# Optimization experiments

Hardware: AMD Instinct MI355X
Metric: run time of the kernel (lower is better)

The kernel has to match this reference:

```python
import jax, jax.numpy as jnp
import numpy as np

B = 16384
FEAT_SIZES = [1000000, 1000000, 500000, 500000, 100000, 100000, 10000, 10000]
EMB_DIM = 50          # min(50, feat_size//2) for all chosen sizes
CONT_IN = 64
D = 8 * EMB_DIM + 64  # 464 = total_embedding_size + 64
H1, H2 = 256, 128     # expert/cross hidden sizes
E, T = 4, 3           # num_experts, num_tasks


def setup_inputs() -> dict:
    key = jax.random.key(0)
    ks = iter(jax.random.split(key, 64))
    s = 0.02
    inp = {}
    inp["discrete_features"] = jax.random.randint(next(ks), (B, 8), 0, 10000)
    inp["continuous_features"] = jax.random.normal(next(ks), (B, CONT_IN), jnp.float32)
    for i, fs in enumerate(FEAT_SIZES):
        inp[f"emb{i}"] = jax.random.normal(next(ks), (fs, EMB_DIM), jnp.float32) * s
    inp["cont_W"] = jax.random.normal(next(ks), (CONT_IN, 64), jnp.float32) * s
    inp["cont_b"] = jnp.zeros((64,), jnp.float32)
    inp["fm_W"] = jax.random.normal(next(ks), (D, 10), jnp.float32) * s
    inp["cW1"] = jax.random.normal(next(ks), (D, H1), jnp.float32) * s
    inp["cb1"] = jnp.zeros((H1,), jnp.float32)
    inp["cW2"] = jax.random.normal(next(ks), (H1, H2), jnp.float32) * s
    inp["cb2"] = jnp.zeros((H2,), jnp.float32)
    inp["coW"] = jax.random.normal(next(ks), (H2, D), jnp.float32) * s
    inp["cob"] = jnp.zeros((D,), jnp.float32)
    inp["expW1"] = jax.random.normal(next(ks), (E, D, H1), jnp.float32) * s
    inp["expb1"] = jnp.zeros((E, H1), jnp.float32)
    inp["expW2"] = jax.random.normal(next(ks), (E, H1, H2), jnp.float32) * s
    inp["expb2"] = jnp.zeros((E, H2), jnp.float32)
    inp["gate_W"] = jax.random.normal(next(ks), (T, D, E), jnp.float32) * s
    inp["gate_b"] = jnp.zeros((T, E), jnp.float32)
    inp["task_W"] = jax.random.normal(next(ks), (T, H2, 1), jnp.float32) * s
    inp["task_b"] = jnp.zeros((T, 1), jnp.float32)
    inp["log_vars"] = jnp.zeros((T,), jnp.float32)
    return inp


def reference(discrete_features, continuous_features,
              emb0, emb1, emb2, emb3, emb4, emb5, emb6, emb7,
              cont_W, cont_b, fm_W, cW1, cb1, cW2, cb2, coW, cob,
              expW1, expb1, expW2, expb2, gate_W, gate_b,
              task_W, task_b, log_vars):
    tables = [emb0, emb1, emb2, emb3, emb4, emb5, emb6, emb7]
    embs = [jnp.take(t, discrete_features[:, i], axis=0) for i, t in enumerate(tables)]
    cont = jax.nn.relu(continuous_features @ cont_W + cont_b)           # [B,64]
    x = jnp.concatenate(embs + [cont], axis=1)                          # [B,D]
    # FM part: x @ fm_embedding.weight -> [B,10], square-of-sum minus sum-of-square
    xe = x @ fm_W
    fm = 0.5 * (jnp.sum(xe, 1, keepdims=True) ** 2
                - jnp.sum(xe ** 2, 1, keepdims=True))                   # [B,1]
    # cross network
    c = jax.nn.relu(x @ cW1 + cb1)
    c = jax.nn.relu(c @ cW2 + cb2)
    co = c @ coW + cob                                                  # [B,D]
    h = x + co + fm                                                     # [B,D] (fm broadcast)
    # experts as batched GEMMs: [B,E,H2]
    e1 = jax.nn.relu(jnp.einsum('bd,edh->beh', h, expW1) + expb1)
    eo = jnp.einsum('beh,eho->beo', e1, expW2) + expb2
    # gates: [B,T,E] softmax over experts
    g = jax.nn.softmax(jnp.einsum('bd,tde->bte', h, gate_W) + gate_b, axis=-1)
    mixed = jnp.einsum('bte,beo->bto', g, eo)                           # [B,T,H2]
    out = jnp.einsum('bto,tok->btk', mixed, task_W) + task_b            # [B,T,1]
    return out[..., 0], log_vars                                        # ([B,3], [3])
```

## Files before the change

### kernel.cpp

```cpp
#include <hip/hip_runtime.h>
#include <stdint.h>

typedef _Float16 f16;
typedef __attribute__((ext_vector_type(8))) _Float16 f16x8;
typedef __attribute__((ext_vector_type(4))) float    f32x4;

constexpr int BROWS = 16384;
constexpr int NTASK = 3;

constexpr int OFF_CW1 = 0;
constexpr int OFF_CW2 = OFF_CW1 + 256 * 480;
constexpr int OFF_COW = OFF_CW2 + 128 * 256;
constexpr int OFF_EW1 = OFF_COW + 512 * 128;
constexpr int OFF_EW2 = OFF_EW1 + 1024 * 480;
constexpr int OFF_FMW = OFF_EW2 + 512 * 256;
constexpr int OFF_GW  = OFF_FMW + 16 * 480;
constexpr int OFF_CTW = OFF_GW  + 16 * 480;
constexpr int PACK_TOTAL = OFF_CTW + 64 * 64;

__global__ __launch_bounds__(256)
void pack_all(const float* __restrict__ cW1, const float* __restrict__ cW2,
              const float* __restrict__ coW, const float* __restrict__ expW1,
              const float* __restrict__ expW2, const float* __restrict__ fmW,
              const float* __restrict__ gateW, const float* __restrict__ contW,
              f16* __restrict__ wp)
{
    const int idx = blockIdx.x * 256 + threadIdx.x;
    if (idx >= PACK_TOTAL) return;
    float v = 0.f;
    if (idx < OFF_CW2) {
        const int l = idx - OFF_CW1, n = l / 480, k = l % 480;
        if (k < 464) v = cW1[k * 256 + n];
    } else if (idx < OFF_COW) {
        const int l = idx - OFF_CW2, n = l / 256, k = l % 256;
        v = cW2[k * 128 + n];
    } else if (idx < OFF_EW1) {
        const int l = idx - OFF_COW, n = l / 128, k = l % 128;
        if (n < 464) v = coW[k * 464 + n];
    } else if (idx < OFF_EW2) {
        const int l = idx - OFF_EW1, n = l / 480, k = l % 480;
        const int e = n >> 8, nn = n & 255;
        if (k < 464) v = expW1[(e * 464 + k) * 256 + nn];
    } else if (idx < OFF_FMW) {
        const int l = idx - OFF_EW2, n = l / 256, k = l % 256;
        const int e = n >> 7, nn = n & 127;
        v = expW2[(e * 256 + k) * 128 + nn];
    } else if (idx < OFF_GW) {
        const int l = idx - OFF_FMW, c = l / 480, k = l % 480;
        if (c < 10 && k < 464) v = fmW[k * 10 + c];
    } else if (idx < OFF_CTW) {
        const int l = idx - OFF_GW, c = l / 480, k = l % 480;
        if (c < 12 && k < 464) {
            const int tt = c >> 2, e = c & 3;
            v = gateW[(tt * 464 + k) * 4 + e];
        }
    } else {
        const int l = idx - OFF_CTW, n = l / 64, k = l % 64;
        v = contW[k * 64 + n];
    }
    wp[idx] = (f16)v;
}

template<int MF, int NF, int KS, int LDA>
__device__ __forceinline__ void wave_gemm(
    const f16* __restrict__ As, int arow0,
    const f16* __restrict__ Bg, int bcol0, int ldb,
    f32x4 (&acc)[MF][NF], int lane)
{
    const int g = lane >> 4, rr = lane & 15;
#pragma unroll
    for (int kb = 0; kb < KS; ++kb) {
        const int ko = kb * 32 + g * 8;
        f16x8 bf[NF];
#pragma unroll
        for (int j = 0; j < NF; ++j)
            bf[j] = *(const f16x8*)(Bg + (long)(bcol0 + j * 16 + rr) * ldb + ko);
#pragma unroll
        for (int i = 0; i < MF; ++i) {
            const f16x8 af = *(const f16x8*)(As + (arow0 + i * 16 + rr) * LDA + ko);
#pragma unroll
            for (int j = 0; j < NF; ++j)
                acc[i][j] = __builtin_amdgcn_mfma_f32_16x16x32_f16(
                    af, bf[j], acc[i][j], 0, 0, 0);
        }
    }
}

__global__ __launch_bounds__(512, 1)
void mmoe_fused(const int* __restrict__ disc, const float* __restrict__ cf,
                const float* __restrict__ e0p, const float* __restrict__ e1p,
                const float* __restrict__ e2p, const float* __restrict__ e3p,
                const float* __restrict__ e4p, const float* __restrict__ e5p,
                const float* __restrict__ e6p, const float* __restrict__ e7p,
                const float* __restrict__ contB, const float* __restrict__ cb1,
                const float* __restrict__ cb2, const float* __restrict__ cob,
                const float* __restrict__ expb1, const float* __restrict__ expb2,
                const float* __restrict__ gateB, const float* __restrict__ taskW,
                const float* __restrict__ taskB, const float* __restrict__ logv,
                const f16* __restrict__ wp, float* __restrict__ out)
{
    __shared__ f16   sh_x [64][488];
    __shared__ f16   sh_c1[64][264];
    __shared__ f16   sh_c2[64][136];
    __shared__ float sh_g [64][12];
    __shared__ float sh_part[8][64][3];
    __shared__ float sh_fm[64];
    __shared__ const float* stabs[8];

    const int t = threadIdx.x;
    const int lane = t & 63, wave = t >> 6;
    const int g = lane >> 4, rr = lane & 15;
    const long r0 = (long)blockIdx.x * 64;

    const f16* cW1p = wp + OFF_CW1;
    const f16* cW2p = wp + OFF_CW2;
    const f16* coWp = wp + OFF_COW;
    const f16* eW1p = wp + OFF_EW1;
    const f16* eW2p = wp + OFF_EW2;
    const f16* fmWp = wp + OFF_FMW;
    const f16* gWp  = wp + OFF_GW;
    const f16* ctWp = wp + OFF_CTW;

    if (t == 0) {
        stabs[0] = e0p; stabs[1] = e1p; stabs[2] = e2p; stabs[3] = e3p;
        stabs[4] = e4p; stabs[5] = e5p; stabs[6] = e6p; stabs[7] = e7p;
    }
    __syncthreads();

    f16* cfp = (f16*)&sh_c2[0][0];
    for (int i = t; i < 64 * 24; i += 512) sh_x[i / 24][464 + i % 24] = (f16)0.f;
    {
        const int r = t >> 3, tab = t & 7;
        const long fi = disc[(r0 + r) * 8 + tab];
        const float* src = stabs[tab] + fi * 50;
        f16* dst = &sh_x[r][tab * 50];
#pragma unroll
        for (int q = 0; q < 25; ++q) {
            const float2 v = *(const float2*)(src + q * 2);
            dst[q * 2] = (f16)v.x; dst[q * 2 + 1] = (f16)v.y;
        }
    }
    for (int i = t; i < 64 * 16; i += 512) {
        const int r = i >> 4, q = i & 15;
        const float4 v = *(const float4*)(cf + (r0 + r) * 64 + q * 4);
        f16* dst = cfp + r * 72 + q * 4;
        dst[0] = (f16)v.x; dst[1] = (f16)v.y; dst[2] = (f16)v.z; dst[3] = (f16)v.w;
    }
    __syncthreads();

    {
        const int wm = wave >> 2, wn = wave & 3;
        f32x4 acc[2][1] = {};
        wave_gemm<2, 1, 2, 72>(cfp, wm * 32, ctWp, wn * 16, 64, acc, lane);
        const int col = wn * 16 + rr;
        const float bv = contB[col];
#pragma unroll
        for (int i = 0; i < 2; ++i)
#pragma unroll
            for (int rx = 0; rx < 4; ++rx)
                sh_x[wm * 32 + i * 16 + g * 4 + rx][400 + col] =
                    (f16)fmaxf(acc[i][0][rx] + bv, 0.f);
    }
    __syncthreads();

    if (wave < 4) {
        f32x4 a[1][1] = {};
        wave_gemm<1, 1, 15, 488>(&sh_x[0][0], wave * 16, fmWp, 0, 480, a, lane);
#pragma unroll
        for (int rx = 0; rx < 4; ++rx) {
            const float v = a[0][0][rx];
            float s = v, ss = v * v;
#pragma unroll
            for (int off = 1; off < 16; off <<= 1) {
                s += __shfl_xor(s, off, 64); ss += __shfl_xor(ss, off, 64);
            }
            if (rr == 0) sh_fm[wave * 16 + g * 4 + rx] = 0.5f * (s * s - ss);
        }
    }
    {
        f32x4 acc[4][2] = {};
        wave_gemm<4, 2, 15, 488>(&sh_x[0][0], 0, cW1p, wave * 32, 480, acc, lane);
#pragma unroll
        for (int j = 0; j < 2; ++j) {
            const int col = wave * 32 + j * 16 + rr;
            const float bv = cb1[col];
#pragma unroll
            for (int i = 0; i < 4; ++i)
#pragma unroll
                for (int rx = 0; rx < 4; ++rx)
                    sh_c1[i * 16 + g * 4 + rx][col] =
                        (f16)fmaxf(acc[i][j][rx] + bv, 0.f);
        }
    }
    __syncthreads();

    {
        f32x4 acc[4][1] = {};
        wave_gemm<4, 1, 8, 264>(&sh_c1[0][0], 0, cW2p, wave * 16, 256, acc, lane);
        const int col = wave * 16 + rr;
        const float bv = cb2[col];
#pragma unroll
        for (int i = 0; i < 4; ++i)
#pragma unroll
            for (int rx = 0; rx < 4; ++rx)
                sh_c2[i * 16 + g * 4 + rx][col] =
                    (f16)fmaxf(acc[i][0][rx] + bv, 0.f);
    }
    __syncthreads();

    {
        f32x4 acc[4][4] = {};
        wave_gemm<4, 4, 4, 136>(&sh_c2[0][0], 0, coWp, wave * 64, 128, acc, lane);
#pragma unroll
        for (int j = 0; j < 4; ++j) {
            const int col = wave * 64 + j * 16 + rr;
            if (col < 464) {
                const float bv = cob[col];
#pragma unroll
                for (int i = 0; i < 4; ++i)
#pragma unroll
                    for (int rx = 0; rx < 4; ++rx) {
                        const int row = i * 16 + g * 4 + rx;
                        const float v = acc[i][j][rx] + bv +
                                        (float)sh_x[row][col] + sh_fm[row];
                        sh_x[row][col] = (f16)v;
                    }
            }
        }
    }
    __syncthreads();

    if (wave < 4) {
        f32x4 a[1][1] = {};
        wave_gemm<1, 1, 15, 488>(&sh_x[0][0], wave * 16, gWp, 0, 480, a, lane);
        const float gb = (rr < 12) ? gateB[rr] : 0.f;
#pragma unroll
        for (int rx = 0; rx < 4; ++rx) {
            const float v = a[0][0][rx] + gb;
            float m = fmaxf(v, __shfl_xor(v, 1, 64));
            m = fmaxf(m, __shfl_xor(m, 2, 64));
            const float p = __expf(v - m);
            float s = p + __shfl_xor(p, 1, 64);
            s += __shfl_xor(s, 2, 64);
            if (rr < 12) sh_g[wave * 16 + g * 4 + rx][rr] = p / s;
        }
    }
    __syncthreads();

    float tw[3];
#pragma unroll
    for (int tt = 0; tt < 3; ++tt) tw[tt] = taskW[tt * 128 + wave * 16 + rr];

    float oacc[4][4][3];
#pragma unroll
    for (int i = 0; i < 4; ++i)
#pragma unroll
        for (int rx = 0; rx < 4; ++rx)
#pragma unroll
            for (int tt = 0; tt < 3; ++tt) oacc[i][rx][tt] = 0.f;

#pragma unroll
    for (int e = 0; e < 4; ++e) {
        {
            f32x4 acc[4][2] = {};
            wave_gemm<4, 2, 15, 488>(&sh_x[0][0], 0, eW1p + e * (256 * 480),
                                     wave * 32, 480, acc, lane);
#pragma unroll
            for (int j = 0; j < 2; ++j) {
                const int col = wave * 32 + j * 16 + rr;
                const float bv = expb1[e * 256 + col];
#pragma unroll
                for (int i = 0; i < 4; ++i)
#pragma unroll
                    for (int rx = 0; rx < 4; ++rx)
                        sh_c1[i * 16 + g * 4 + rx][col] =
                            (f16)fmaxf(acc[i][j][rx] + bv, 0.f);
            }
        }
        __syncthreads();
        {
            f32x4 acc[4][1] = {};
            wave_gemm<4, 1, 8, 264>(&sh_c1[0][0], 0, eW2p + e * (128 * 256),
                                    wave * 16, 256, acc, lane);
            const float bv = expb2[e * 128 + wave * 16 + rr];
#pragma unroll
            for (int i = 0; i < 4; ++i)
#pragma unroll
                for (int rx = 0; rx < 4; ++rx) {
                    const int row = i * 16 + g * 4 + rx;
                    const float v0 = acc[i][0][rx] + bv;
#pragma unroll
                    for (int tt = 0; tt < 3; ++tt)
                        oacc[i][rx][tt] += sh_g[row][tt * 4 + e] * (v0 * tw[tt]);
                }
        }
        __syncthreads();
    }

#pragma unroll
    for (int i = 0; i < 4; ++i)
#pragma unroll
        for (int rx = 0; rx < 4; ++rx)
#pragma unroll
            for (int tt = 0; tt < 3; ++tt) {
                float s = oacc[i][rx][tt];
#pragma unroll
                for (int off = 1; off < 16; off <<= 1)
                    s += __shfl_xor(s, off, 64);
                if (rr == 0)
                    sh_part[wave][i * 16 + g * 4 + rx][tt] = s;
            }
    __syncthreads();
    if (t < 64 * 3) {
        const int row = t / 3, tt = t - row * 3;
        float s = taskB[tt];
#pragma unroll
        for (int w = 0; w < 8; ++w) s += sh_part[w][row][tt];
        out[(r0 + row) * 3 + tt] = s;
    }
    if (blockIdx.x == 0 && t < NTASK) out[(long)BROWS * 3 + t] = logv[t];
}

extern "C" void kernel_launch(void* const* d_in, const int* in_sizes, int n_in,
                              void* d_out, int out_size, void* d_ws, size_t ws_size,
                              hipStream_t stream)
{
    (void)in_sizes; (void)n_in; (void)out_size; (void)ws_size;

    const int*   disc  = (const int*)  d_in[0];
    const float* cf    = (const float*)d_in[1];
    const float* emb0  = (const float*)d_in[2];
    const float* emb1  = (const float*)d_in[3];
    const float* emb2  = (const float*)d_in[4];
    const float* emb3  = (const float*)d_in[5];
    const float* emb4  = (const float*)d_in[6];
    const float* emb5  = (const float*)d_in[7];
    const float* emb6  = (const float*)d_in[8];
    const float* emb7  = (const float*)d_in[9];
    const float* contW = (const float*)d_in[10];
    const float* contB = (const float*)d_in[11];
    const float* fmW   = (const float*)d_in[12];
    const float* cW1   = (const float*)d_in[13];
    const float* cb1   = (const float*)d_in[14];
    const float* cW2   = (const float*)d_in[15];
    const float* cb2   = (const float*)d_in[16];
    const float* coW   = (const float*)d_in[17];
    const float* cob   = (const float*)d_in[18];
    const float* expW1 = (const float*)d_in[19];
    const float* expb1 = (const float*)d_in[20];
    const float* expW2 = (const float*)d_in[21];
    const float* expb2 = (const float*)d_in[22];
    const float* gateW = (const float*)d_in[23];
    const float* gateB = (const float*)d_in[24];
    const float* taskW = (const float*)d_in[25];
    const float* taskB = (const float*)d_in[26];
    const float* logv  = (const float*)d_in[27];

    f16* wp = (f16*)d_ws;

    pack_all<<<(PACK_TOTAL + 255) / 256, 256, 0, stream>>>(
        cW1, cW2, coW, expW1, expW2, fmW, gateW, contW, wp);

    mmoe_fused<<<BROWS / 64, 512, 0, stream>>>(
        disc, cf, emb0, emb1, emb2, emb3, emb4, emb5, emb6, emb7,
        contB, cb1, cb2, cob, expb1, expb2, gateB, taskW, taskB, logv,
        wp, (float*)d_out);
}
```

Before: 106.5 us.

## Process 128 rows per block with split hidden halves and staggered weight access

Each block now handles 128 rows instead of 64, so every weight tile fetched from global memory feeds twice as many rows. To fit this in LDS, the 256-wide hidden layers are computed in two 128-column halves that share a single buffer, with accumulation carried in registers. K-loop start offsets and the expert order are rotated per block to spread weight reads across memory, and gate values are stored in f16. The cost is that the grid drops to 128 blocks, which may leave many CUs idle, and more barriers are needed per stage.

```diff
diff --git a/kernel.cpp b/kernel.cpp
--- a/kernel.cpp
+++ b/kernel.cpp
@@ -6,7 +6,6 @@
 typedef __attribute__((ext_vector_type(4))) float    f32x4;
 
 constexpr int BROWS = 16384;
-constexpr int NTASK = 3;
 
 constexpr int OFF_CW1 = 0;
 constexpr int OFF_CW2 = OFF_CW1 + 256 * 480;
@@ -65,12 +64,13 @@
 __device__ __forceinline__ void wave_gemm(
     const f16* __restrict__ As, int arow0,
     const f16* __restrict__ Bg, int bcol0, int ldb,
-    f32x4 (&acc)[MF][NF], int lane)
+    f32x4 (&acc)[MF][NF], int lane, int rot)
 {
     const int g = lane >> 4, rr = lane & 15;
 #pragma unroll
     for (int kb = 0; kb < KS; ++kb) {
-        const int ko = kb * 32 + g * 8;
+        int kk = kb + rot; if (kk >= KS) kk -= KS;
+        const int ko = kk * 32 + g * 8;
         f16x8 bf[NF];
 #pragma unroll
         for (int j = 0; j < NF; ++j)
@@ -86,7 +86,7 @@
     }
 }
 
-__global__ __launch_bounds__(512, 1)
+__global__ __launch_bounds__(512, 2)
 void mmoe_fused(const int* __restrict__ disc, const float* __restrict__ cf,
                 const float* __restrict__ e0p, const float* __restrict__ e1p,
                 const float* __restrict__ e2p, const float* __restrict__ e3p,
@@ -99,18 +99,19 @@
                 const float* __restrict__ taskB, const float* __restrict__ logv,
                 const f16* __restrict__ wp, float* __restrict__ out)
 {
-    __shared__ f16   sh_x [64][488];
-    __shared__ f16   sh_c1[64][264];
-    __shared__ f16   sh_c2[64][136];
-    __shared__ float sh_g [64][12];
-    __shared__ float sh_part[8][64][3];
-    __shared__ float sh_fm[64];
+    __shared__ f16   sh_x  [128][488];
+    __shared__ f16   sh_buf[128][136];
+    __shared__ f16   sh_g  [128][12];
+    __shared__ float sh_fm [128];
     __shared__ const float* stabs[8];
 
     const int t = threadIdx.x;
     const int lane = t & 63, wave = t >> 6;
     const int g = lane >> 4, rr = lane & 15;
-    const long r0 = (long)blockIdx.x * 64;
+    const int bid = blockIdx.x;
+    const int r0 = bid * 128;
+    const int rot15 = (bid >> 3) % 15;
+    const int rot4  = (bid >> 3) & 3;
 
     const f16* cW1p = wp + OFF_CW1;
     const f16* cW2p = wp + OFF_CW2;
@@ -127,10 +128,10 @@
     }
     __syncthreads();
 
-    f16* cfp = (f16*)&sh_c2[0][0];
-    for (int i = t; i < 64 * 24; i += 512) sh_x[i / 24][464 + i % 24] = (f16)0.f;
-    {
-        const int r = t >> 3, tab = t & 7;
+    for (int i = t; i < 128 * 24; i += 512) sh_x[i / 24][464 + i % 24] = (f16)0.f;
+#pragma unroll
+    for (int p = t; p < 1024; p += 512) {
+        const int r = p >> 3, tab = p & 7;
         const long fi = disc[(r0 + r) * 8 + tab];
         const float* src = stabs[tab] + fi * 50;
         f16* dst = &sh_x[r][tab * 50];
@@ -140,32 +141,32 @@
             dst[q * 2] = (f16)v.x; dst[q * 2 + 1] = (f16)v.y;
         }
     }
-    for (int i = t; i < 64 * 16; i += 512) {
+    for (int i = t; i < 128 * 16; i += 512) {
         const int r = i >> 4, q = i & 15;
-        const float4 v = *(const float4*)(cf + (r0 + r) * 64 + q * 4);
-        f16* dst = cfp + r * 72 + q * 4;
+        const float4 v = *(const float4*)(cf + (long)(r0 + r) * 64 + q * 4);
+        f16* dst = &sh_buf[r][q * 4];
         dst[0] = (f16)v.x; dst[1] = (f16)v.y; dst[2] = (f16)v.z; dst[3] = (f16)v.w;
     }
     __syncthreads();
 
     {
         const int wm = wave >> 2, wn = wave & 3;
-        f32x4 acc[2][1] = {};
-        wave_gemm<2, 1, 2, 72>(cfp, wm * 32, ctWp, wn * 16, 64, acc, lane);
+        f32x4 acc[4][1] = {};
+        wave_gemm<4, 1, 2, 136>(&sh_buf[0][0], wm * 64, ctWp, wn * 16, 64, acc, lane, 0);
         const int col = wn * 16 + rr;
         const float bv = contB[col];
 #pragma unroll
-        for (int i = 0; i < 2; ++i)
+        for (int i = 0; i < 4; ++i)
 #pragma unroll
             for (int rx = 0; rx < 4; ++rx)
-                sh_x[wm * 32 + i * 16 + g * 4 + rx][400 + col] =
+                sh_x[wm * 64 + i * 16 + g * 4 + rx][400 + col] =
                     (f16)fmaxf(acc[i][0][rx] + bv, 0.f);
     }
     __syncthreads();
 
-    if (wave < 4) {
+    {
         f32x4 a[1][1] = {};
-        wave_gemm<1, 1, 15, 488>(&sh_x[0][0], wave * 16, fmWp, 0, 480, a, lane);
+        wave_gemm<1, 1, 15, 488>(&sh_x[0][0], wave * 16, fmWp, 0, 480, a, lane, rot15);
 #pragma unroll
         for (int rx = 0; rx < 4; ++rx) {
             const float v = a[0][0][rx];
@@ -178,39 +179,51 @@
         }
     }
     {
-        f32x4 acc[4][2] = {};
-        wave_gemm<4, 2, 15, 488>(&sh_x[0][0], 0, cW1p, wave * 32, 480, acc, lane);
-#pragma unroll
-        for (int j = 0; j < 2; ++j) {
-            const int col = wave * 32 + j * 16 + rr;
-            const float bv = cb1[col];
-#pragma unroll
-            for (int i = 0; i < 4; ++i)
-#pragma unroll
-                for (int rx = 0; rx < 4; ++rx)
-                    sh_c1[i * 16 + g * 4 + rx][col] =
-                        (f16)fmaxf(acc[i][j][rx] + bv, 0.f);
-        }
-    }
-    __syncthreads();
-
-    {
-        f32x4 acc[4][1] = {};
-        wave_gemm<4, 1, 8, 264>(&sh_c1[0][0], 0, cW2p, wave * 16, 256, acc, lane);
+        f32x4 acc[8][1] = {};
+        wave_gemm<8, 1, 15, 488>(&sh_x[0][0], 0, cW1p, wave * 16, 480, acc, lane, rot15);
+        const int col = wave * 16 + rr;
+        const float bv = cb1[col];
+#pragma unroll
+        for (int i = 0; i < 8; ++i)
+#pragma unroll
+            for (int rx = 0; rx < 4; ++rx)
+                sh_buf[i * 16 + g * 4 + rx][col] = (f16)fmaxf(acc[i][0][rx] + bv, 0.f);
+    }
+    __syncthreads();
+
+    f32x4 c2acc[8][1] = {};
+    wave_gemm<8, 1, 4, 136>(&sh_buf[0][0], 0, cW2p, wave * 16, 256, c2acc, lane, rot4);
+    __syncthreads();
+    {
+        f32x4 acc[8][1] = {};
+        wave_gemm<8, 1, 15, 488>(&sh_x[0][0], 0, cW1p, 128 + wave * 16, 480, acc, lane, rot15);
+        const int col = wave * 16 + rr;
+        const float bv = cb1[128 + col];
+        __syncthreads();
+#pragma unroll
+        for (int i = 0; i < 8; ++i)
+#pragma unroll
+            for (int rx = 0; rx < 4; ++rx)
+                sh_buf[i * 16 + g * 4 + rx][col] = (f16)fmaxf(acc[i][0][rx] + bv, 0.f);
+    }
+    __syncthreads();
+    wave_gemm<8, 1, 4, 136>(&sh_buf[0][0], 0, cW2p + 128, wave * 16, 256, c2acc, lane, rot4);
+    __syncthreads();
+    {
         const int col = wave * 16 + rr;
         const float bv = cb2[col];
 #pragma unroll
-        for (int i = 0; i < 4; ++i)
+        for (int i = 0; i < 8; ++i)
 #pragma unroll
             for (int rx = 0; rx < 4; ++rx)
-                sh_c2[i * 16 + g * 4 + rx][col] =
-                    (f16)fmaxf(acc[i][0][rx] + bv, 0.f);
-    }
-    __syncthreads();
-
-    {
+                sh_buf[i * 16 + g * 4 + rx][col] = (f16)fmaxf(c2acc[i][0][rx] + bv, 0.f);
+    }
+    __syncthreads();
+
+#pragma unroll
+    for (int half = 0; half < 2; ++half) {
         f32x4 acc[4][4] = {};
-        wave_gemm<4, 4, 4, 136>(&sh_c2[0][0], 0, coWp, wave * 64, 128, acc, lane);
+        wave_gemm<4, 4, 4, 136>(&sh_buf[0][0], half * 64, coWp, wave * 64, 128, acc, lane, rot4);
 #pragma unroll
         for (int j = 0; j < 4; ++j) {
             const int col = wave * 64 + j * 16 + rr;
@@ -220,7 +233,7 @@
                 for (int i = 0; i < 4; ++i)
 #pragma unroll
                     for (int rx = 0; rx < 4; ++rx) {
-                        const int row = i * 16 + g * 4 + rx;
+                        const int row = half * 64 + i * 16 + g * 4 + rx;
                         const float v = acc[i][j][rx] + bv +
                                         (float)sh_x[row][col] + sh_fm[row];
                         sh_x[row][col] = (f16)v;
@@ -230,9 +243,9 @@
     }
     __syncthreads();
 
-    if (wave < 4) {
+    {
         f32x4 a[1][1] = {};
-        wave_gemm<1, 1, 15, 488>(&sh_x[0][0], wave * 16, gWp, 0, 480, a, lane);
+        wave_gemm<1, 1, 15, 488>(&sh_x[0][0], wave * 16, gWp, 0, 480, a, lane, rot15);
         const float gb = (rr < 12) ? gateB[rr] : 0.f;
 #pragma unroll
         for (int rx = 0; rx < 4; ++rx) {
@@ -242,63 +255,78 @@
             const float p = __expf(v - m);
             float s = p + __shfl_xor(p, 1, 64);
             s += __shfl_xor(s, 2, 64);
-            if (rr < 12) sh_g[wave * 16 + g * 4 + rx][rr] = p / s;
-        }
-    }
-    __syncthreads();
+            if (rr < 12) sh_g[wave * 16 + g * 4 + rx][rr] = (f16)(p / s);
+        }
+    }
 
     float tw[3];
 #pragma unroll
     for (int tt = 0; tt < 3; ++tt) tw[tt] = taskW[tt * 128 + wave * 16 + rr];
 
-    float oacc[4][4][3];
-#pragma unroll
-    for (int i = 0; i < 4; ++i)
+    float oacc[8][4][3];
+#pragma unroll
+    for (int i = 0; i < 8; ++i)
 #pragma unroll
         for (int rx = 0; rx < 4; ++rx)
 #pragma unroll
             for (int tt = 0; tt < 3; ++tt) oacc[i][rx][tt] = 0.f;
 
-#pragma unroll
+#pragma unroll 1
     for (int e = 0; e < 4; ++e) {
+        const int ee = (e + bid) & 3;
         {
-            f32x4 acc[4][2] = {};
-            wave_gemm<4, 2, 15, 488>(&sh_x[0][0], 0, eW1p + e * (256 * 480),
-                                     wave * 32, 480, acc, lane);
-#pragma unroll
-            for (int j = 0; j < 2; ++j) {
-                const int col = wave * 32 + j * 16 + rr;
-                const float bv = expb1[e * 256 + col];
-#pragma unroll
-                for (int i = 0; i < 4; ++i)
-#pragma unroll
-                    for (int rx = 0; rx < 4; ++rx)
-                        sh_c1[i * 16 + g * 4 + rx][col] =
-                            (f16)fmaxf(acc[i][j][rx] + bv, 0.f);
-            }
-        }
+            f32x4 acc[8][1] = {};
+            wave_gemm<8, 1, 15, 488>(&sh_x[0][0], 0, eW1p, ee * 256 + wave * 16, 480,
+                                     acc, lane, rot15);
+            const int col = wave * 16 + rr;
+            const float bv = expb1[ee * 256 + col];
+            __syncthreads();
+#pragma unroll
+            for (int i = 0; i < 8; ++i)
+#pragma unroll
+                for (int rx = 0; rx < 4; ++rx)
+                    sh_buf[i * 16 + g * 4 + rx][col] = (f16)fmaxf(acc[i][0][rx] + bv, 0.f);
+        }
+        __syncthreads();
+        f32x4 eacc[8][1] = {};
+        wave_gemm<8, 1, 4, 136>(&sh_buf[0][0], 0, eW2p, ee * 128 + wave * 16, 256,
+                                eacc, lane, rot4);
         __syncthreads();
         {
-            f32x4 acc[4][1] = {};
-            wave_gemm<4, 1, 8, 264>(&sh_c1[0][0], 0, eW2p + e * (128 * 256),
-                                    wave * 16, 256, acc, lane);
-            const float bv = expb2[e * 128 + wave * 16 + rr];
-#pragma unroll
-            for (int i = 0; i < 4; ++i)
+            f32x4 acc[8][1] = {};
+            wave_gemm<8, 1, 15, 488>(&sh_x[0][0], 0, eW1p, ee * 256 + 128 + wave * 16, 480,
+                                     acc, lane, rot15);
+            const int col = wave * 16 + rr;
+            const float bv = expb1[ee * 256 + 128 + col];
+            __syncthreads();
+#pragma unroll
+            for (int i = 0; i < 8; ++i)
+#pragma unroll
+                for (int rx = 0; rx < 4; ++rx)
+                    sh_buf[i * 16 + g * 4 + rx][col] = (f16)fmaxf(acc[i][0][rx] + bv, 0.f);
+        }
+        __syncthreads();
+        wave_gemm<8, 1, 4, 136>(&sh_buf[0][0], 0, eW2p + 128, ee * 128 + wave * 16, 256,
+                                eacc, lane, rot4);
+        {
+            const float bv = expb2[ee * 128 + wave * 16 + rr];
+#pragma unroll
+            for (int i = 0; i < 8; ++i)
 #pragma unroll
                 for (int rx = 0; rx < 4; ++rx) {
                     const int row = i * 16 + g * 4 + rx;
-                    const float v0 = acc[i][0][rx] + bv;
+                    const float v = eacc[i][0][rx] + bv;
 #pragma unroll
                     for (int tt = 0; tt < 3; ++tt)
-                        oacc[i][rx][tt] += sh_g[row][tt * 4 + e] * (v0 * tw[tt]);
+                        oacc[i][rx][tt] += (float)sh_g[row][tt * 4 + ee] * (v * tw[tt]);
                 }
         }
         __syncthreads();
     }
 
-#pragma unroll
-    for (int i = 0; i < 4; ++i)
+    float* sh_part = (float*)&sh_buf[0][0];
+#pragma unroll
+    for (int i = 0; i < 8; ++i)
 #pragma unroll
         for (int rx = 0; rx < 4; ++rx)
 #pragma unroll
@@ -308,17 +336,17 @@
                 for (int off = 1; off < 16; off <<= 1)
                     s += __shfl_xor(s, off, 64);
                 if (rr == 0)
-                    sh_part[wave][i * 16 + g * 4 + rx][tt] = s;
+                    sh_part[(wave * 128 + i * 16 + g * 4 + rx) * 3 + tt] = s;
             }
     __syncthreads();
-    if (t < 64 * 3) {
+    if (t < 128 * 3) {
         const int row = t / 3, tt = t - row * 3;
         float s = taskB[tt];
 #pragma unroll
-        for (int w = 0; w < 8; ++w) s += sh_part[w][row][tt];
-        out[(r0 + row) * 3 + tt] = s;
-    }
-    if (blockIdx.x == 0 && t < NTASK) out[(long)BROWS * 3 + t] = logv[t];
+        for (int w = 0; w < 8; ++w) s += sh_part[(w * 128 + row) * 3 + tt];
+        out[(long)(r0 + row) * 3 + tt] = s;
+    }
+    if (bid == 0 && t < 3) out[(long)BROWS * 3 + t] = logv[t];
 }
 
 extern "C" void kernel_launch(void* const* d_in, const int* in_sizes, int n_in,
@@ -361,7 +389,7 @@
     pack_all<<<(PACK_TOTAL + 255) / 256, 256, 0, stream>>>(
         cW1, cW2, coW, expW1, expW2, fmW, gateW, contW, wp);
 
-    mmoe_fused<<<BROWS / 64, 512, 0, stream>>>(
+    mmoe_fused<<<BROWS / 128, 512, 0, stream>>>(
         disc, cf, emb0, emb1, emb2, emb3, emb4, emb5, emb6, emb7,
         contB, cb1, cb2, cob, expb1, expb2, gateB, taskW, taskB, logv,
         wp, (float*)d_out);
```

New measurement: 171.1 us. 60.6% more time.

## Stage weight slabs through double-buffered LDS and fold FM/gate GEMMs into wider GEMMs

Applied to the files above, without the earlier changes.

Each weight GEMM now copies 32-wide K slabs of the packed weights into two LDS buffers with global_load_lds, prefetching the next slab while MFMAs run on the current one. Before, every wave read B fragments straight from global memory on its own. The FM projection is packed as extra columns of the cross-layer W1, and the gate projection as extra columns of expert 0's W1. This removes the separate small GEMM passes and some barriers, and the launch bound changes to (512,2). The cost is a __syncthreads per K step, some wasted MFMA columns for the waves that do not need the extra columns, and higher LDS use that likely still caps occupancy at one block per CU.

```diff
diff --git a/kernel.cpp b/kernel.cpp
--- a/kernel.cpp
+++ b/kernel.cpp
@@ -6,17 +6,21 @@
 typedef __attribute__((ext_vector_type(4))) float    f32x4;
 
 constexpr int BROWS = 16384;
-constexpr int NTASK = 3;
-
-constexpr int OFF_CW1 = 0;
-constexpr int OFF_CW2 = OFF_CW1 + 256 * 480;
-constexpr int OFF_COW = OFF_CW2 + 128 * 256;
-constexpr int OFF_EW1 = OFF_COW + 512 * 128;
-constexpr int OFF_EW2 = OFF_EW1 + 1024 * 480;
-constexpr int OFF_FMW = OFF_EW2 + 512 * 256;
-constexpr int OFF_GW  = OFF_FMW + 16 * 480;
-constexpr int OFF_CTW = OFF_GW  + 16 * 480;
+
+constexpr int OFF_CW1F = 0;
+constexpr int OFF_CW2  = OFF_CW1F + 272 * 480;
+constexpr int OFF_COW  = OFF_CW2  + 128 * 256;
+constexpr int OFF_EW1G = OFF_COW  + 512 * 128;
+constexpr int OFF_EW2  = OFF_EW1G + 1040 * 480;
+constexpr int OFF_CTW  = OFF_EW2  + 512 * 256;
 constexpr int PACK_TOTAL = OFF_CTW + 64 * 64;
+
+__device__ __forceinline__ void g2l16(const void* g, void* l) {
+    __builtin_amdgcn_global_load_lds(
+        (__attribute__((address_space(1))) void*)(void*)g,
+        (__attribute__((address_space(3))) void*)l,
+        16, 0, 0);
+}
 
 __global__ __launch_bounds__(256)
 void pack_all(const float* __restrict__ cW1, const float* __restrict__ cW2,
@@ -29,31 +33,31 @@
     if (idx >= PACK_TOTAL) return;
     float v = 0.f;
     if (idx < OFF_CW2) {
-        const int l = idx - OFF_CW1, n = l / 480, k = l % 480;
-        if (k < 464) v = cW1[k * 256 + n];
+        const int l = idx, n = l / 480, k = l % 480;
+        if (n < 256) { if (k < 464) v = cW1[k * 256 + n]; }
+        else { const int c = n - 256; if (c < 10 && k < 464) v = fmW[k * 10 + c]; }
     } else if (idx < OFF_COW) {
         const int l = idx - OFF_CW2, n = l / 256, k = l % 256;
         v = cW2[k * 128 + n];
-    } else if (idx < OFF_EW1) {
+    } else if (idx < OFF_EW1G) {
         const int l = idx - OFF_COW, n = l / 128, k = l % 128;
         if (n < 464) v = coW[k * 464 + n];
     } else if (idx < OFF_EW2) {
-        const int l = idx - OFF_EW1, n = l / 480, k = l % 480;
-        const int e = n >> 8, nn = n & 255;
-        if (k < 464) v = expW1[(e * 464 + k) * 256 + nn];
-    } else if (idx < OFF_FMW) {
+        const int l = idx - OFF_EW1G, n = l / 480, k = l % 480;
+        if (n < 272) {
+            if (n < 256) { if (k < 464) v = expW1[(long)k * 256 + n]; }
+            else {
+                const int c = n - 256;
+                if (c < 12 && k < 464) v = gateW[((c >> 2) * 464 + k) * 4 + (c & 3)];
+            }
+        } else {
+            const int m = n - 272, e = 1 + m / 256, nn = m % 256;
+            if (k < 464) v = expW1[((long)e * 464 + k) * 256 + nn];
+        }
+    } else if (idx < OFF_CTW) {
         const int l = idx - OFF_EW2, n = l / 256, k = l % 256;
         const int e = n >> 7, nn = n & 127;
         v = expW2[(e * 256 + k) * 128 + nn];
-    } else if (idx < OFF_GW) {
-        const int l = idx - OFF_FMW, c = l / 480, k = l % 480;
-        if (c < 10 && k < 464) v = fmW[k * 10 + c];
-    } else if (idx < OFF_CTW) {
-        const int l = idx - OFF_GW, c = l / 480, k = l % 480;
-        if (c < 12 && k < 464) {
-            const int tt = c >> 2, e = c & 3;
-            v = gateW[(tt * 464 + k) * 4 + e];
-        }
     } else {
         const int l = idx - OFF_CTW, n = l / 64, k = l % 64;
         v = contW[k * 64 + n];
@@ -61,32 +65,68 @@
     wp[idx] = (f16)v;
 }
 
-template<int MF, int NF, int KS, int LDA>
-__device__ __forceinline__ void wave_gemm(
-    const f16* __restrict__ As, int arow0,
-    const f16* __restrict__ Bg, int bcol0, int ldb,
-    f32x4 (&acc)[MF][NF], int lane)
+template<int NCOLS>
+__device__ __forceinline__ void stage_slab(const f16* __restrict__ Bk, int ldb,
+                                           f16* slab, int wave, int lane)
+{
+    constexpr int SLOTS = NCOLS * 4;
+    constexpr int FULL  = SLOTS / 512;
+    constexpr int REM   = SLOTS % 512;
+#pragma unroll
+    for (int p = 0; p < FULL; ++p) {
+        const int sp = p * 512 + wave * 64 + lane;
+        g2l16(Bk + (long)(sp >> 2) * ldb + (sp & 3) * 8,
+              slab + (size_t)(p * 512 + wave * 64) * 8);
+    }
+    if constexpr (REM > 0) {
+        if (wave < REM / 64) {
+            const int sp = FULL * 512 + wave * 64 + lane;
+            g2l16(Bk + (long)(sp >> 2) * ldb + (sp & 3) * 8,
+                  slab + (size_t)(FULL * 512 + wave * 64) * 8);
+        }
+    }
+}
+
+template<int MF, int NF, int LDA>
+__device__ __forceinline__ void mfma_step(
+    const f16* __restrict__ As, const f16* __restrict__ slab,
+    int bcol0, int k0, f32x4 (&acc)[MF][NF], int g, int rr)
+{
+    f16x8 bf[NF];
+#pragma unroll
+    for (int j = 0; j < NF; ++j)
+        bf[j] = *(const f16x8*)(slab + (size_t)((bcol0 + j * 16 + rr) * 4 + g) * 8);
+#pragma unroll
+    for (int i = 0; i < MF; ++i) {
+        const f16x8 af = *(const f16x8*)(As + (size_t)(i * 16 + rr) * LDA + k0 + g * 8);
+#pragma unroll
+        for (int j = 0; j < NF; ++j)
+            acc[i][j] = __builtin_amdgcn_mfma_f32_16x16x32_f16(
+                af, bf[j], acc[i][j], 0, 0, 0);
+    }
+}
+
+template<int MF, int NF, int NCOLS, int KS, int LDA>
+__device__ __forceinline__ void gemm_pipe(
+    const f16* __restrict__ As, const f16* __restrict__ Bg, int ldb,
+    f16* slab0, f16* slab1, int bcol0,
+    f32x4 (&acc)[MF][NF], int wave, int lane)
 {
     const int g = lane >> 4, rr = lane & 15;
+    stage_slab<NCOLS>(Bg, ldb, slab0, wave, lane);
 #pragma unroll
     for (int kb = 0; kb < KS; ++kb) {
-        const int ko = kb * 32 + g * 8;
-        f16x8 bf[NF];
-#pragma unroll
-        for (int j = 0; j < NF; ++j)
-            bf[j] = *(const f16x8*)(Bg + (long)(bcol0 + j * 16 + rr) * ldb + ko);
-#pragma unroll
-        for (int i = 0; i < MF; ++i) {
-            const f16x8 af = *(const f16x8*)(As + (arow0 + i * 16 + rr) * LDA + ko);
-#pragma unroll
-            for (int j = 0; j < NF; ++j)
-                acc[i][j] = __builtin_amdgcn_mfma_f32_16x16x32_f16(
-                    af, bf[j], acc[i][j], 0, 0, 0);
-        }
-    }
-}
-
-__global__ __launch_bounds__(512, 1)
+        __syncthreads();
+        if (kb + 1 < KS)
+            stage_slab<NCOLS>(Bg + (kb + 1) * 32, ldb,
+                              (kb & 1) ? slab0 : slab1, wave, lane);
+        mfma_step<MF, NF, LDA>(As, (kb & 1) ? slab1 : slab0, bcol0,
+                               kb * 32, acc, g, rr);
+    }
+    __syncthreads();
+}
+
+__global__ __launch_bounds__(512, 2)
 void mmoe_fused(const int* __restrict__ disc, const float* __restrict__ cf,
                 const float* __restrict__ e0p, const float* __restrict__ e1p,
                 const float* __restrict__ e2p, const float* __restrict__ e3p,
@@ -99,9 +139,10 @@
                 const float* __restrict__ taskB, const float* __restrict__ logv,
                 const f16* __restrict__ wp, float* __restrict__ out)
 {
-    __shared__ f16   sh_x [64][488];
-    __shared__ f16   sh_c1[64][264];
-    __shared__ f16   sh_c2[64][136];
+    __shared__ __align__(16) f16 sh_x [64][488];
+    __shared__ __align__(16) f16 sh_c1[64][264];
+    __shared__ __align__(16) f16 sh_c2[64][136];
+    __shared__ __align__(16) f16 slab[2][272 * 32];
     __shared__ float sh_g [64][12];
     __shared__ float sh_part[8][64][3];
     __shared__ float sh_fm[64];
@@ -111,15 +152,6 @@
     const int lane = t & 63, wave = t >> 6;
     const int g = lane >> 4, rr = lane & 15;
     const long r0 = (long)blockIdx.x * 64;
-
-    const f16* cW1p = wp + OFF_CW1;
-    const f16* cW2p = wp + OFF_CW2;
-    const f16* coWp = wp + OFF_COW;
-    const f16* eW1p = wp + OFF_EW1;
-    const f16* eW2p = wp + OFF_EW2;
-    const f16* fmWp = wp + OFF_FMW;
-    const f16* gWp  = wp + OFF_GW;
-    const f16* ctWp = wp + OFF_CTW;
 
     if (t == 0) {
         stabs[0] = e0p; stabs[1] = e1p; stabs[2] = e2p; stabs[3] = e3p;
@@ -150,8 +182,19 @@
 
     {
         const int wm = wave >> 2, wn = wave & 3;
-        f32x4 acc[2][1] = {};
-        wave_gemm<2, 1, 2, 72>(cfp, wm * 32, ctWp, wn * 16, 64, acc, lane);
+        const f16* ctW = wp + OFF_CTW;
+        f32x4 acc[2];
+        acc[0] = (f32x4){0.f, 0.f, 0.f, 0.f}; acc[1] = acc[0];
+#pragma unroll
+        for (int kb = 0; kb < 2; ++kb) {
+            const int ko = kb * 32 + g * 8;
+            const f16x8 bfv = *(const f16x8*)(ctW + (size_t)(wn * 16 + rr) * 64 + ko);
+#pragma unroll
+            for (int i = 0; i < 2; ++i) {
+                const f16x8 af = *(const f16x8*)(cfp + (size_t)(wm * 32 + i * 16 + rr) * 72 + ko);
+                acc[i] = __builtin_amdgcn_mfma_f32_16x16x32_f16(af, bfv, acc[i], 0, 0, 0);
+            }
+        }
         const int col = wn * 16 + rr;
         const float bv = contB[col];
 #pragma unroll
@@ -159,27 +202,13 @@
 #pragma unroll
             for (int rx = 0; rx < 4; ++rx)
                 sh_x[wm * 32 + i * 16 + g * 4 + rx][400 + col] =
-                    (f16)fmaxf(acc[i][0][rx] + bv, 0.f);
-    }
-    __syncthreads();
-
-    if (wave < 4) {
-        f32x4 a[1][1] = {};
-        wave_gemm<1, 1, 15, 488>(&sh_x[0][0], wave * 16, fmWp, 0, 480, a, lane);
-#pragma unroll
-        for (int rx = 0; rx < 4; ++rx) {
-            const float v = a[0][0][rx];
-            float s = v, ss = v * v;
-#pragma unroll
-            for (int off = 1; off < 16; off <<= 1) {
-                s += __shfl_xor(s, off, 64); ss += __shfl_xor(ss, off, 64);
-            }
-            if (rr == 0) sh_fm[wave * 16 + g * 4 + rx] = 0.5f * (s * s - ss);
-        }
-    }
+                    (f16)fmaxf(acc[i][rx] + bv, 0.f);
+    }
+
     {
-        f32x4 acc[4][2] = {};
-        wave_gemm<4, 2, 15, 488>(&sh_x[0][0], 0, cW1p, wave * 32, 480, acc, lane);
+        f32x4 acc[4][3] = {};
+        gemm_pipe<4, 3, 272, 15, 488>(&sh_x[0][0], wp + OFF_CW1F, 480,
+                                      slab[0], slab[1], wave * 32, acc, wave, lane);
 #pragma unroll
         for (int j = 0; j < 2; ++j) {
             const int col = wave * 32 + j * 16 + rr;
@@ -191,12 +220,27 @@
                     sh_c1[i * 16 + g * 4 + rx][col] =
                         (f16)fmaxf(acc[i][j][rx] + bv, 0.f);
         }
-    }
-    __syncthreads();
+        if (wave == 7) {
+#pragma unroll
+            for (int i = 0; i < 4; ++i)
+#pragma unroll
+                for (int rx = 0; rx < 4; ++rx) {
+                    const float v = (rr < 10) ? acc[i][2][rx] : 0.f;
+                    float s = v, ss = v * v;
+#pragma unroll
+                    for (int off = 1; off < 16; off <<= 1) {
+                        s += __shfl_xor(s, off, 64); ss += __shfl_xor(ss, off, 64);
+                    }
+                    if (rr == 0)
+                        sh_fm[i * 16 + g * 4 + rx] = 0.5f * (s * s - ss);
+                }
+        }
+    }
 
     {
         f32x4 acc[4][1] = {};
-        wave_gemm<4, 1, 8, 264>(&sh_c1[0][0], 0, cW2p, wave * 16, 256, acc, lane);
+        gemm_pipe<4, 1, 128, 8, 264>(&sh_c1[0][0], wp + OFF_CW2, 256,
+                                     slab[0], slab[1], wave * 16, acc, wave, lane);
         const int col = wave * 16 + rr;
         const float bv = cb2[col];
 #pragma unroll
@@ -206,14 +250,15 @@
                 sh_c2[i * 16 + g * 4 + rx][col] =
                     (f16)fmaxf(acc[i][0][rx] + bv, 0.f);
     }
-    __syncthreads();
-
-    {
-        f32x4 acc[4][4] = {};
-        wave_gemm<4, 4, 4, 136>(&sh_c2[0][0], 0, coWp, wave * 64, 128, acc, lane);
-#pragma unroll
-        for (int j = 0; j < 4; ++j) {
-            const int col = wave * 64 + j * 16 + rr;
+
+#pragma unroll 1
+    for (int half = 0; half < 2; ++half) {
+        f32x4 acc[4][2] = {};
+        gemm_pipe<4, 2, 256, 4, 136>(&sh_c2[0][0], wp + OFF_COW + half * 256 * 128, 128,
+                                     slab[0], slab[1], wave * 32, acc, wave, lane);
+#pragma unroll
+        for (int j = 0; j < 2; ++j) {
+            const int col = half * 256 + wave * 32 + j * 16 + rr;
             if (col < 464) {
                 const float bv = cob[col];
 #pragma unroll
@@ -228,29 +273,10 @@
             }
         }
     }
-    __syncthreads();
-
-    if (wave < 4) {
-        f32x4 a[1][1] = {};
-        wave_gemm<1, 1, 15, 488>(&sh_x[0][0], wave * 16, gWp, 0, 480, a, lane);
-        const float gb = (rr < 12) ? gateB[rr] : 0.f;
-#pragma unroll
-        for (int rx = 0; rx < 4; ++rx) {
-            const float v = a[0][0][rx] + gb;
-            float m = fmaxf(v, __shfl_xor(v, 1, 64));
-            m = fmaxf(m, __shfl_xor(m, 2, 64));
-            const float p = __expf(v - m);
-            float s = p + __shfl_xor(p, 1, 64);
-            s += __shfl_xor(s, 2, 64);
-            if (rr < 12) sh_g[wave * 16 + g * 4 + rx][rr] = p / s;
-        }
-    }
-    __syncthreads();
 
     float tw[3];
 #pragma unroll
     for (int tt = 0; tt < 3; ++tt) tw[tt] = taskW[tt * 128 + wave * 16 + rr];
-
     float oacc[4][4][3];
 #pragma unroll
     for (int i = 0; i < 4; ++i)
@@ -259,12 +285,44 @@
 #pragma unroll
             for (int tt = 0; tt < 3; ++tt) oacc[i][rx][tt] = 0.f;
 
-#pragma unroll
+#pragma unroll 1
     for (int e = 0; e < 4; ++e) {
-        {
+        if (e == 0) {
+            f32x4 acc[4][3] = {};
+            gemm_pipe<4, 3, 272, 15, 488>(&sh_x[0][0], wp + OFF_EW1G, 480,
+                                          slab[0], slab[1], wave * 32, acc, wave, lane);
+#pragma unroll
+            for (int j = 0; j < 2; ++j) {
+                const int col = wave * 32 + j * 16 + rr;
+                const float bv = expb1[col];
+#pragma unroll
+                for (int i = 0; i < 4; ++i)
+#pragma unroll
+                    for (int rx = 0; rx < 4; ++rx)
+                        sh_c1[i * 16 + g * 4 + rx][col] =
+                            (f16)fmaxf(acc[i][j][rx] + bv, 0.f);
+            }
+            if (wave == 7) {
+                const float gb = (rr < 12) ? gateB[rr] : 0.f;
+#pragma unroll
+                for (int i = 0; i < 4; ++i)
+#pragma unroll
+                    for (int rx = 0; rx < 4; ++rx) {
+                        const float v = acc[i][2][rx] + gb;
+                        float m = fmaxf(v, __shfl_xor(v, 1, 64));
+                        m = fmaxf(m, __shfl_xor(m, 2, 64));
+                        const float p = __expf(v - m);
+                        float s = p + __shfl_xor(p, 1, 64);
+                        s += __shfl_xor(s, 2, 64);
+                        if (rr < 12)
+                            sh_g[i * 16 + g * 4 + rx][rr] = p / s;
+                    }
+            }
+        } else {
             f32x4 acc[4][2] = {};
-            wave_gemm<4, 2, 15, 488>(&sh_x[0][0], 0, eW1p + e * (256 * 480),
-                                     wave * 32, 480, acc, lane);
+            gemm_pipe<4, 2, 256, 15, 488>(
+                &sh_x[0][0], wp + OFF_EW1G + (size_t)(272 + (e - 1) * 256) * 480, 480,
+                slab[0], slab[1], wave * 32, acc, wave, lane);
 #pragma unroll
             for (int j = 0; j < 2; ++j) {
                 const int col = wave * 32 + j * 16 + rr;
@@ -277,24 +335,22 @@
                             (f16)fmaxf(acc[i][j][rx] + bv, 0.f);
             }
         }
-        __syncthreads();
         {
             f32x4 acc[4][1] = {};
-            wave_gemm<4, 1, 8, 264>(&sh_c1[0][0], 0, eW2p + e * (128 * 256),
-                                    wave * 16, 256, acc, lane);
+            gemm_pipe<4, 1, 128, 8, 264>(&sh_c1[0][0], wp + OFF_EW2 + (size_t)e * 128 * 256, 256,
+                                         slab[0], slab[1], wave * 16, acc, wave, lane);
             const float bv = expb2[e * 128 + wave * 16 + rr];
 #pragma unroll
             for (int i = 0; i < 4; ++i)
 #pragma unroll
                 for (int rx = 0; rx < 4; ++rx) {
                     const int row = i * 16 + g * 4 + rx;
-                    const float v0 = acc[i][0][rx] + bv;
+                    const float v = acc[i][0][rx] + bv;
 #pragma unroll
                     for (int tt = 0; tt < 3; ++tt)
-                        oacc[i][rx][tt] += sh_g[row][tt * 4 + e] * (v0 * tw[tt]);
+                        oacc[i][rx][tt] += sh_g[row][tt * 4 + e] * (v * tw[tt]);
                 }
         }
-        __syncthreads();
     }
 
 #pragma unroll
@@ -318,7 +374,7 @@
         for (int w = 0; w < 8; ++w) s += sh_part[w][row][tt];
         out[(r0 + row) * 3 + tt] = s;
     }
-    if (blockIdx.x == 0 && t < NTASK) out[(long)BROWS * 3 + t] = logv[t];
+    if (blockIdx.x == 0 && t < 3) out[(long)BROWS * 3 + t] = logv[t];
 }
 
 extern "C" void kernel_launch(void* const* d_in, const int* in_sizes, int n_in,
```

New measurement: 112.1 us. 1.05x slower.
